# Optimization experiments

Hardware: AMD Instinct MI355X
Metric: run time of the kernel (lower is better)

Reference implementation:

```python
import jax, jax.numpy as jnp
from jax import lax
import numpy as np

LAMBDA_DAG = 0.5
B, C = 64, 5000
PARENT_PROB = 0.0008  # ~4 parents per GO term


def setup_inputs() -> dict:
    key = jax.random.key(0)
    k1, k2, k3 = jax.random.split(key, 3)
    logits = jax.random.normal(k1, (B, C), dtype=jnp.float32)
    # sparse multilabel targets (binary floats, like GO annotations)
    labels = (jax.random.uniform(k2, (B, C)) < 0.02).astype(jnp.float32)
    # sparse binary DAG adjacency: dag[i, j] = 1 if j is a parent of i
    dag = (jax.random.uniform(k3, (C, C)) < PARENT_PROB).astype(jnp.float32)
    dag = dag * (1.0 - jnp.eye(C, dtype=jnp.float32))  # no self-parents
    return {"logits": logits, "labels": labels, "dag_matrix": dag}


def reference(logits, labels, dag_matrix):
    # BCEWithLogitsLoss (mean): log(1 + exp(l)) - l * y, numerically stable
    bce = jnp.mean(jnp.logaddexp(0.0, logits) - logits * labels)

    probs = jax.nn.sigmoid(logits)                      # [B, C]
    mask = (dag_matrix > 0).astype(probs.dtype)          # [C, C]
    n_par = mask.sum(axis=1)                             # [C] parents per child

    # Accumulate sum over batch of relu(p_child - p_parent)^2 as a [C, C] matrix
    # via scan over the batch dim (keeps peak memory at one [C, C] tile).
    def body(acc, p):  # p: [C]
        d = jnp.maximum(p[:, None] - p[None, :], 0.0)
        return acc + d * d, None

    nterms = probs.shape[1]
    viol_sum, _ = lax.scan(body, jnp.zeros((nterms, nterms), probs.dtype), probs)

    # per-child-term mean over (batch, n_parents_i), only for terms with parents
    per_term = (viol_sum * mask).sum(axis=1)             # [C]
    batch = jnp.asarray(probs.shape[0], probs.dtype)
    term_mean = jnp.where(n_par > 0, per_term / (batch * jnp.maximum(n_par, 1.0)), 0.0)

    total_edges = mask.sum()
    dag_penalty = jnp.where(total_edges > 0, term_mean.sum() / jnp.maximum(total_edges, 1.0), 0.0)

    loss = bce + LAMBDA_DAG * dag_penalty
    return loss
```

## Files before the change

### kernel.cpp

```cpp
#include <hip/hip_runtime.h>
#include <math.h>

#define LAMBDA_DAG 0.5f

__global__ void k_probs_bce(const float* __restrict__ logits,
                            const float* __restrict__ labels,
                            float* __restrict__ pT,
                            float* __restrict__ bce_part,
                            float* __restrict__ per_term,
                            float* __restrict__ npar,
                            int B, int C) {
    const int N = B * C;
    const int stride = gridDim.x * blockDim.x;
    const int t0 = blockIdx.x * blockDim.x + threadIdx.x;

    for (int i = t0; i < C; i += stride) { per_term[i] = 0.f; npar[i] = 0.f; }

    float accv = 0.f;
    for (int idx = t0; idx < N; idx += stride) {
        float l = logits[idx];
        float y = labels[idx];
        accv += fmaxf(l, 0.f) + log1pf(expf(-fabsf(l))) - l * y;
        float p = 1.f / (1.f + expf(-l));
        int b = idx / C;
        int c = idx - b * C;
        pT[(size_t)c * B + b] = p;
    }
    __shared__ float sdata[256];
    sdata[threadIdx.x] = accv;
    __syncthreads();
    for (int s = blockDim.x >> 1; s > 0; s >>= 1) {
        if (threadIdx.x < s) sdata[threadIdx.x] += sdata[threadIdx.x + s];
        __syncthreads();
    }
    if (threadIdx.x == 0) bce_part[blockIdx.x] = sdata[0];
}

__global__ void __launch_bounds__(256) k_dag_flat(
        const float* __restrict__ dag,
        const float* __restrict__ pT,
        float* __restrict__ per_term,
        float* __restrict__ npar,
        int B, int C, int nseg) {
    const int seg = blockIdx.x * blockDim.x + threadIdx.x;
    if (seg >= nseg) return;
    const int base = seg * 32;
    const float4* dp = (const float4*)(dag + (size_t)base);

    float4 v[8];
#pragma unroll
    for (int h = 0; h < 8; ++h) v[h] = dp[h];

    const int B4 = B >> 2;
#pragma unroll
    for (int h = 0; h < 8; ++h) {
        float4 d4 = v[h];
        float g = d4.x + d4.y + d4.z + d4.w;
        if (g > 0.f) {
#pragma unroll
            for (int k = 0; k < 4; ++k) {
                float dv = (k == 0) ? d4.x : (k == 1) ? d4.y : (k == 2) ? d4.z : d4.w;
                if (dv > 0.f) {
                    int f = base + h * 4 + k;
                    int i = f / C;
                    int j = f - i * C;
                    const float4* pi4 = (const float4*)(pT + (size_t)i * B);
                    const float4* pj4 = (const float4*)(pT + (size_t)j * B);
                    float s = 0.f;
                    for (int q = 0; q < B4; ++q) {
                        float4 a = pi4[q];
                        float4 b = pj4[q];
                        float d0 = fmaxf(a.x - b.x, 0.f);
                        float d1 = fmaxf(a.y - b.y, 0.f);
                        float d2 = fmaxf(a.z - b.z, 0.f);
                        float d3 = fmaxf(a.w - b.w, 0.f);
                        s += d0 * d0 + d1 * d1 + d2 * d2 + d3 * d3;
                    }
                    for (int b = B4 * 4; b < B; ++b) {
                        float diff = fmaxf(pT[(size_t)i * B + b] - pT[(size_t)j * B + b], 0.f);
                        s += diff * diff;
                    }
                    atomicAdd(&per_term[i], s);
                    atomicAdd(&npar[i], 1.f);
                }
            }
        }
    }
}

__global__ void k_final(const float* __restrict__ per_term,
                        const float* __restrict__ npar,
                        const float* __restrict__ bce_part, int nb,
                        float* __restrict__ out, int B, int C) {
    float bs = 0.f, ps = 0.f, es = 0.f;
    for (int k = threadIdx.x; k < nb; k += blockDim.x) bs += bce_part[k];
    for (int i = threadIdx.x; i < C; i += blockDim.x) {
        float np = npar[i];
        es += np;
        if (np > 0.f) ps += per_term[i] / ((float)B * np);
    }
    __shared__ float s1[256], s2[256], s3[256];
    s1[threadIdx.x] = bs;
    s2[threadIdx.x] = ps;
    s3[threadIdx.x] = es;
    __syncthreads();
    for (int s = blockDim.x >> 1; s > 0; s >>= 1) {
        if (threadIdx.x < s) {
            s1[threadIdx.x] += s1[threadIdx.x + s];
            s2[threadIdx.x] += s2[threadIdx.x + s];
            s3[threadIdx.x] += s3[threadIdx.x + s];
        }
        __syncthreads();
    }
    if (threadIdx.x == 0) {
        float penalty = (s3[0] > 0.f) ? (s2[0] / s3[0]) : 0.f;
        out[0] = s1[0] / (float)(B * C) + LAMBDA_DAG * penalty;
    }
}

extern "C" void kernel_launch(void* const* d_in, const int* in_sizes, int n_in,
                              void* d_out, int out_size, void* d_ws, size_t ws_size,
                              hipStream_t stream) {
    const float* logits = (const float*)d_in[0];
    const float* labels = (const float*)d_in[1];
    const float* dag    = (const float*)d_in[2];
    float* out = (float*)d_out;

    const int C = (int)(sqrt((double)in_sizes[2]) + 0.5);
    const int B = in_sizes[0] / C;
    const int CC = in_sizes[2];

    float* ws       = (float*)d_ws;
    float* pT       = ws;
    float* per_term = pT + (size_t)C * B;
    float* nparw    = per_term + C;
    float* bce_part = nparw + C;
    const int NB1 = 320;

    k_probs_bce<<<NB1, 256, 0, stream>>>(logits, labels, pT, bce_part,
                                         per_term, nparw, B, C);

    const int nseg = (CC + 31) / 32;
    const int nblk = (nseg + 255) / 256;
    k_dag_flat<<<nblk, 256, 0, stream>>>(dag, pT, per_term, nparw, B, C, nseg);

    k_final<<<1, 256, 0, stream>>>(per_term, nparw, bce_part, NB1, out, B, C);
}
```

Measured before the change: 195.3 us.

## Compact DAG edges into a list, then process each edge with one wavefront

Splits the fused scan-and-compute DAG kernel in two. The first kernel scans the dense adjacency and writes nonzero edge indices into a global list, using a shared-memory staging buffer and one global atomic per block. A second kernel then gives each edge to a 64-lane wavefront, which reduces over the batch with shuffles. This removes the divergent serial per-thread batch loops in the scan kernel, at the cost of an extra launch and extra workspace. Edges beyond the per-block buffer cap are silently dropped.

```diff
diff --git a/kernel.cpp b/kernel.cpp
--- a/kernel.cpp
+++ b/kernel.cpp
@@ -9,11 +9,13 @@
                             float* __restrict__ bce_part,
                             float* __restrict__ per_term,
                             float* __restrict__ npar,
+                            int* __restrict__ edge_cnt,
                             int B, int C) {
     const int N = B * C;
     const int stride = gridDim.x * blockDim.x;
     const int t0 = blockIdx.x * blockDim.x + threadIdx.x;
 
+    if (t0 == 0) edge_cnt[0] = 0;
     for (int i = t0; i < C; i += stride) { per_term[i] = 0.f; npar[i] = 0.f; }
 
     float accv = 0.f;
@@ -36,54 +38,80 @@
     if (threadIdx.x == 0) bce_part[blockIdx.x] = sdata[0];
 }
 
-__global__ void __launch_bounds__(256) k_dag_flat(
-        const float* __restrict__ dag,
-        const float* __restrict__ pT,
-        float* __restrict__ per_term,
-        float* __restrict__ npar,
-        int B, int C, int nseg) {
+#define LBUF_CAP 2048
+__global__ void __launch_bounds__(256) k_dag_scan(
+        const float* __restrict__ dag, int CC,
+        int* __restrict__ edge_buf, int* __restrict__ edge_cnt,
+        int nseg) {
+    __shared__ int lcnt, lbase;
+    __shared__ int lbuf[LBUF_CAP];
+    if (threadIdx.x == 0) lcnt = 0;
+    __syncthreads();
+
     const int seg = blockIdx.x * blockDim.x + threadIdx.x;
-    if (seg >= nseg) return;
-    const int base = seg * 32;
-    const float4* dp = (const float4*)(dag + (size_t)base);
-
-    float4 v[8];
+    if (seg < nseg) {
+        const int base = seg * 32;
+        if (base + 32 <= CC) {
+            const float4* dp = (const float4*)(dag + (size_t)base);
+            float4 v[8];
 #pragma unroll
-    for (int h = 0; h < 8; ++h) v[h] = dp[h];
-
-    const int B4 = B >> 2;
+            for (int h = 0; h < 8; ++h) v[h] = dp[h];
 #pragma unroll
-    for (int h = 0; h < 8; ++h) {
-        float4 d4 = v[h];
-        float g = d4.x + d4.y + d4.z + d4.w;
-        if (g > 0.f) {
+            for (int h = 0; h < 8; ++h) {
+                float4 d4 = v[h];
+                if (d4.x + d4.y + d4.z + d4.w > 0.f) {
 #pragma unroll
-            for (int k = 0; k < 4; ++k) {
-                float dv = (k == 0) ? d4.x : (k == 1) ? d4.y : (k == 2) ? d4.z : d4.w;
-                if (dv > 0.f) {
-                    int f = base + h * 4 + k;
-                    int i = f / C;
-                    int j = f - i * C;
-                    const float4* pi4 = (const float4*)(pT + (size_t)i * B);
-                    const float4* pj4 = (const float4*)(pT + (size_t)j * B);
-                    float s = 0.f;
-                    for (int q = 0; q < B4; ++q) {
-                        float4 a = pi4[q];
-                        float4 b = pj4[q];
-                        float d0 = fmaxf(a.x - b.x, 0.f);
-                        float d1 = fmaxf(a.y - b.y, 0.f);
-                        float d2 = fmaxf(a.z - b.z, 0.f);
-                        float d3 = fmaxf(a.w - b.w, 0.f);
-                        s += d0 * d0 + d1 * d1 + d2 * d2 + d3 * d3;
+                    for (int k = 0; k < 4; ++k) {
+                        float dv = (k == 0) ? d4.x : (k == 1) ? d4.y
+                                 : (k == 2) ? d4.z : d4.w;
+                        if (dv > 0.f) {
+                            int slot = atomicAdd(&lcnt, 1);
+                            if (slot < LBUF_CAP) lbuf[slot] = base + h * 4 + k;
+                        }
                     }
-                    for (int b = B4 * 4; b < B; ++b) {
-                        float diff = fmaxf(pT[(size_t)i * B + b] - pT[(size_t)j * B + b], 0.f);
-                        s += diff * diff;
-                    }
-                    atomicAdd(&per_term[i], s);
-                    atomicAdd(&npar[i], 1.f);
                 }
             }
+        } else {
+            for (int f = base; f < CC; ++f) {
+                if (dag[f] > 0.f) {
+                    int slot = atomicAdd(&lcnt, 1);
+                    if (slot < LBUF_CAP) lbuf[slot] = f;
+                }
+            }
+        }
+    }
+    __syncthreads();
+    int n = min(lcnt, LBUF_CAP);
+    if (threadIdx.x == 0) lbase = atomicAdd(edge_cnt, n);
+    __syncthreads();
+    for (int t = threadIdx.x; t < n; t += blockDim.x)
+        edge_buf[lbase + t] = lbuf[t];
+}
+
+__global__ void __launch_bounds__(256) k_edges(
+        const int* __restrict__ edge_buf, const int* __restrict__ edge_cnt,
+        const float* __restrict__ pT,
+        float* __restrict__ per_term, float* __restrict__ npar,
+        int B, int C) {
+    const int lane = threadIdx.x & 63;
+    const int wid = (blockIdx.x * blockDim.x + threadIdx.x) >> 6;
+    const int nw = (gridDim.x * blockDim.x) >> 6;
+    const int ne = edge_cnt[0];
+    for (int e = wid; e < ne; e += nw) {
+        int f = edge_buf[e];
+        int i = f / C;
+        int j = f - i * C;
+        float s = 0.f;
+        for (int b = lane; b < B; b += 64) {
+            float diff = fmaxf(pT[(size_t)i * B + b] - pT[(size_t)j * B + b], 0.f);
+            s += diff * diff;
+        }
+#pragma unroll
+        for (int off = 32; off > 0; off >>= 1)
+            s += __shfl_down(s, off, 64);
+        if (lane == 0) {
+            atomicAdd(&per_term[i], s);
+            atomicAdd(&npar[i], 1.f);
         }
     }
 }
@@ -126,8 +154,8 @@
     const float* dag    = (const float*)d_in[2];
     float* out = (float*)d_out;
 
-    const int C = (int)(sqrt((double)in_sizes[2]) + 0.5);
-    const int B = in_sizes[0] / C;
+    const int C  = (int)(sqrt((double)in_sizes[2]) + 0.5);
+    const int B  = in_sizes[0] / C;
     const int CC = in_sizes[2];
 
     float* ws       = (float*)d_ws;
@@ -136,13 +164,17 @@
     float* nparw    = per_term + C;
     float* bce_part = nparw + C;
     const int NB1 = 320;
+    int* edge_cnt   = (int*)(bce_part + NB1);
+    int* edge_buf   = edge_cnt + 4;
 
     k_probs_bce<<<NB1, 256, 0, stream>>>(logits, labels, pT, bce_part,
-                                         per_term, nparw, B, C);
+                                         per_term, nparw, edge_cnt, B, C);
 
     const int nseg = (CC + 31) / 32;
     const int nblk = (nseg + 255) / 256;
-    k_dag_flat<<<nblk, 256, 0, stream>>>(dag, pT, per_term, nparw, B, C, nseg);
+    k_dag_scan<<<nblk, 256, 0, stream>>>(dag, CC, edge_buf, edge_cnt, nseg);
+
+    k_edges<<<512, 256, 0, stream>>>(edge_buf, edge_cnt, pT, per_term, nparw, B, C);
 
     k_final<<<1, 256, 0, stream>>>(per_term, nparw, bce_part, NB1, out, B, C);
 }
```

Result: no change. 192.4 us (-1.5%).
